# Performance work log

Hardware: AMD Instinct MI355X
Metric: run time of the kernel (lower is better)

The kernel has to match this reference:

```python
import jax, jax.numpy as jnp
import numpy as np

DIM = 256
HEADS = 8
SPLIT = 7
IDX = 0  # H_sp = H, W_sp = split_size
SCALE = (DIM // HEADS) ** -0.5


def setup_inputs() -> dict:
    key = jax.random.key(0)
    k1, k2, k3 = jax.random.split(key, 3)
    B, H, W = 16, 56, 56
    L = H * W
    qkv = jax.random.normal(k1, (3, B, L, DIM), jnp.float32)
    get_v_w = jax.random.normal(k2, (DIM, 1, 3, 3), jnp.float32) * 0.1
    get_v_b = jax.random.normal(k3, (DIM,), jnp.float32) * 0.1
    return {"qkv": qkv, "get_v_w": get_v_w, "get_v_b": get_v_b, "H": H, "W": W}


def reference(qkv, get_v_w, get_v_b, H, W):
    q, k, v = qkv[0], qkv[1], qkv[2]
    B, L, C = q.shape
    Hs, Ws = H, SPLIT  # idx == 0 branch
    hd = C // HEADS
    win = Hs * Ws
    nW = B * (H // Hs) * (W // Ws)

    def im2cswin(x):
        x = x.reshape(B, H // Hs, Hs, W // Ws, Ws, C)
        x = x.transpose(0, 1, 3, 2, 4, 5).reshape(nW, win, HEADS, hd)
        return x.transpose(0, 2, 1, 3)

    qw = im2cswin(q) * SCALE
    kw = im2cswin(k)

    # LePE: depthwise 3x3 conv applied per window in NCHW layout
    vimg = v.reshape(B, H // Hs, Hs, W // Ws, Ws, C)
    vimg = vimg.transpose(0, 1, 3, 5, 2, 4).reshape(nW, C, Hs, Ws)
    lepe = jax.lax.conv_general_dilated(
        vimg, get_v_w, window_strides=(1, 1), padding='SAME',
        feature_group_count=C,
        dimension_numbers=('NCHW', 'OIHW', 'NCHW'))
    lepe = lepe + get_v_b[None, :, None, None]
    lepe = lepe.reshape(nW, HEADS, hd, win).transpose(0, 1, 3, 2)
    vw = vimg.reshape(nW, HEADS, hd, win).transpose(0, 1, 3, 2)

    attn = jax.nn.softmax(jnp.einsum('whqd,whkd->whqk', qw, kw), axis=-1)
    x = jnp.einsum('whqk,whkd->whqd', attn, vw) + lepe

    # windows -> image -> [B, L, C]
    x = x.transpose(0, 2, 1, 3).reshape(B, H // Hs, W // Ws, Hs, Ws, C)
    x = x.transpose(0, 1, 3, 2, 4, 5).reshape(B, H * W, C)
    return x
```

## Files before the change

### kernel.cpp

```cpp
#include <hip/hip_runtime.h>
#include <hip/hip_bf16.h>


#define NB    16
#define IMGH  56
#define IMGW  56
#define LTOK  3136
#define DIMC  256
#define NHEAD 8
#define HD    32
#define WS    7
#define WIN   392
#define QS    0.17677669529663687f
#define LOG2E 1.4426950408889634f

#define KROWS  416
#define KPITCH 40
#define VPITCH 424
#define NKT    13
#define NQT    13

typedef __attribute__((ext_vector_type(8)))  short short8;
typedef __attribute__((ext_vector_type(16))) float f32x16;

union U4S8 { unsigned u[4]; short8 v; };

__device__ inline short f2bf(float x) {
    __hip_bfloat16 h = __float2bfloat16(x);
    union { __hip_bfloat16 b; short s; } u; u.b = h; return u.s;
}
__device__ inline float bf2f(short s) {
    union { float f; unsigned u; } u;
    u.u = ((unsigned)(unsigned short)s) << 16; return u.f;
}
__device__ inline unsigned pk2(float a, float b) {
    return (unsigned)(unsigned short)f2bf(a) | ((unsigned)(unsigned short)f2bf(b) << 16);
}

#if __has_builtin(__builtin_amdgcn_exp2f)
__device__ inline float exp2v(float x) { return __builtin_amdgcn_exp2f(x); }
#else
__device__ inline float exp2v(float x) {
    float r; asm("v_exp_f32 %0, %1" : "=v"(r) : "v"(x)); return r;
}
#endif

__device__ inline void plswap(unsigned &a, unsigned &b) {
    asm("s_nop 1\n\tv_permlane32_swap_b32 %0, %1" : "+v"(a), "+v"(b));
}
__device__ inline void plswapf(float &a, float &b) {
    asm("s_nop 1\n\tv_permlane32_swap_b32 %0, %1" : "+v"(a), "+v"(b));
}

__global__ __launch_bounds__(512, 4) void lepe_mfma_kernel(
    const float* __restrict__ qkv,
    const float* __restrict__ w9,
    const float* __restrict__ bias,
    float* __restrict__ out)
{
    const int tid  = threadIdx.x;
    const int lane = tid & 63;
    const int wave = tid >> 6;
    const int blk  = blockIdx.x;
    const int hh   = blk & 7;
    const int wi   = blk >> 3;
    const int b    = wi >> 3;
    const int wb   = wi & 7;

    __shared__ __align__(16) short Kb[KROWS * KPITCH];
    __shared__ __align__(16) short Vt[HD * VPITCH];
    __shared__ float Ws9[HD][9];
    __shared__ float Bs[HD];
    __shared__ float InvAll[KROWS];

    {
        const int sub = tid & 7;
        const int rb  = tid >> 3;
        for (int it = 0; it < 7; ++it) {
            const int r = it * 64 + rb;
            if (r < WIN) {
                const int h = r / WS, w = r - h * WS;
                const int l = h * IMGW + wb * WS + w;
                const size_t kb = ((size_t)(NB + b) * LTOK + l) * DIMC + hh * HD + sub * 4;
                const float4 kq = *(const float4*)(qkv + kb);
                const float4 vq = *(const float4*)(qkv + kb + (size_t)NB * LTOK * DIMC);
                short4 ks;
                ks.x = f2bf(kq.x); ks.y = f2bf(kq.y); ks.z = f2bf(kq.z); ks.w = f2bf(kq.w);
                *(short4*)&Kb[r * KPITCH + sub * 4] = ks;
                const int d0 = sub * 4;
                Vt[(d0 + 0) * VPITCH + r] = f2bf(vq.x);
                Vt[(d0 + 1) * VPITCH + r] = f2bf(vq.y);
                Vt[(d0 + 2) * VPITCH + r] = f2bf(vq.z);
                Vt[(d0 + 3) * VPITCH + r] = f2bf(vq.w);
            } else if (r < KROWS) {
                *(short4*)&Kb[r * KPITCH + sub * 4] = make_short4(0, 0, 0, 0);
            }
        }
        for (int i = tid; i < HD * (VPITCH - WIN); i += 512) {
            const int d = i >> 5;
            const int c = WIN + (i & 31);
            Vt[d * VPITCH + c] = 0;
        }
        for (int i = tid; i < HD * 9; i += 512)
            Ws9[i / 9][i % 9] = w9[(hh * HD + i / 9) * 9 + (i % 9)];
        if (tid < HD) Bs[tid] = bias[hh * HD + tid];
    }
    __syncthreads();

    const int cq = lane & 31;
    const int hi = lane >> 5;

    f32x16 accA, accB;

    auto attn = [&](int qt, f32x16 &acc) {
        int qtok = qt * 32 + cq; if (qtok > WIN - 1) qtok = WIN - 1;
        const int qh = qtok / WS, qw = qtok - qh * WS;
        const int ql = qh * IMGW + wb * WS + qw;
        const float* qp = qkv + ((size_t)b * LTOK + ql) * DIMC + hh * HD;
        const float qs = QS * LOG2E;
        const float4 qa = *(const float4*)(qp + hi * 8);
        const float4 qb = *(const float4*)(qp + hi * 8 + 4);
        const float4 qc = *(const float4*)(qp + 16 + hi * 8);
        const float4 qd = *(const float4*)(qp + 16 + hi * 8 + 4);
        U4S8 qf0, qf1;
        qf0.u[0] = pk2(qa.x * qs, qa.y * qs);
        qf0.u[1] = pk2(qa.z * qs, qa.w * qs);
        qf0.u[2] = pk2(qb.x * qs, qb.y * qs);
        qf0.u[3] = pk2(qb.z * qs, qb.w * qs);
        qf1.u[0] = pk2(qc.x * qs, qc.y * qs);
        qf1.u[1] = pk2(qc.z * qs, qc.w * qs);
        qf1.u[2] = pk2(qd.x * qs, qd.y * qs);
        qf1.u[3] = pk2(qd.z * qs, qd.w * qs);

        #pragma unroll
        for (int i = 0; i < 16; ++i) acc[i] = 0.f;
        float lsum = 0.f;

        for (int kt = 0; kt < NKT - 1; ++kt) {
            const short* kr = &Kb[(kt * 32 + cq) * KPITCH];
            const short8 ka0 = *(const short8*)(kr + hi * 8);
            const short8 ka1 = *(const short8*)(kr + 16 + hi * 8);
            const short* vr = &Vt[cq * VPITCH + kt * 32 + hi * 8];
            const short8 vb0 = *(const short8*)vr;
            const short8 vb1 = *(const short8*)(vr + 16);

            f32x16 S;
            #pragma unroll
            for (int i = 0; i < 16; ++i) S[i] = 0.f;
            S = __builtin_amdgcn_mfma_f32_32x32x16_bf16(ka0, qf0.v, S, 0, 0, 0);
            S = __builtin_amdgcn_mfma_f32_32x32x16_bf16(ka1, qf1.v, S, 0, 0, 0);

            float p[16];
            #pragma unroll
            for (int r = 0; r < 16; ++r) { p[r] = exp2v(S[r]); lsum += p[r]; }

            unsigned u0 = pk2(p[0],  p[1]),  u2 = pk2(p[4],  p[5]);
            unsigned u1 = pk2(p[2],  p[3]),  u3 = pk2(p[6],  p[7]);
            plswap(u0, u2);
            plswap(u1, u3);
            U4S8 pa0; pa0.u[0] = u0; pa0.u[1] = u1; pa0.u[2] = u2; pa0.u[3] = u3;
            acc = __builtin_amdgcn_mfma_f32_32x32x16_bf16(pa0.v, vb0, acc, 0, 0, 0);

            unsigned t0 = pk2(p[8],  p[9]),  t2 = pk2(p[12], p[13]);
            unsigned t1 = pk2(p[10], p[11]), t3 = pk2(p[14], p[15]);
            plswap(t0, t2);
            plswap(t1, t3);
            U4S8 pa1; pa1.u[0] = t0; pa1.u[1] = t1; pa1.u[2] = t2; pa1.u[3] = t3;
            acc = __builtin_amdgcn_mfma_f32_32x32x16_bf16(pa1.v, vb1, acc, 0, 0, 0);
        }

        {
            const int kt = NKT - 1;
            const short* kr = &Kb[(kt * 32 + cq) * KPITCH];
            const short8 ka0 = *(const short8*)(kr + hi * 8);
            const short8 ka1 = *(const short8*)(kr + 16 + hi * 8);
            const short* vr = &Vt[cq * VPITCH + kt * 32 + hi * 8];
            const short8 vb0 = *(const short8*)vr;

            f32x16 S;
            #pragma unroll
            for (int i = 0; i < 16; ++i) S[i] = 0.f;
            S = __builtin_amdgcn_mfma_f32_32x32x16_bf16(ka0, qf0.v, S, 0, 0, 0);
            S = __builtin_amdgcn_mfma_f32_32x32x16_bf16(ka1, qf1.v, S, 0, 0, 0);

            const float p0 = exp2v(S[0]), p1 = exp2v(S[1]);
            const float p2 = exp2v(S[2]), p3 = exp2v(S[3]);
            lsum += (p0 + p1) + (p2 + p3);
            unsigned u0 = pk2(p0, p1), u2 = 0u;
            unsigned u1 = pk2(p2, p3), u3 = 0u;
            plswap(u0, u2);
            plswap(u1, u3);
            U4S8 pa0; pa0.u[0] = u0; pa0.u[1] = u1; pa0.u[2] = u2; pa0.u[3] = u3;
            acc = __builtin_amdgcn_mfma_f32_32x32x16_bf16(pa0.v, vb0, acc, 0, 0, 0);
        }

        float s0 = lsum, s1 = lsum;
        plswapf(s0, s1);
        const float inv = 1.0f / (s0 + s1);
        if (hi == 0) InvAll[qt * 32 + cq] = inv;
    };

    attn(wave, accA);
    const int qtB = wave + 8;
    if (qtB < NQT) attn(qtB, accB);
    __syncthreads();

    short* Vs = Kb;
    for (int i = tid; i < WIN * HD; i += 512) {
        const int d = i & 31, t = i >> 5;
        Vs[t * HD + d] = Vt[d * VPITCH + t];
    }
    __syncthreads();

    auto epi = [&](int qt, f32x16 &acc) {
        #pragma unroll
        for (int r = 0; r < 16; ++r) {
            const int qrow = (r & 3) + 8 * (r >> 2) + 4 * hi;
            const int ot = qt * 32 + qrow;
            if (ot < WIN) {
                const float invr = InvAll[ot];
                const int h = ot / WS, w = ot - h * WS;
                float lp = Bs[cq];
                #pragma unroll
                for (int dy = -1; dy <= 1; ++dy) {
                    const int hy = h + dy;
                    if ((unsigned)hy >= (unsigned)IMGH) continue;
                    #pragma unroll
                    for (int dx = -1; dx <= 1; ++dx) {
                        const int wx = w + dx;
                        if ((unsigned)wx >= (unsigned)WS) continue;
                        lp += bf2f(Vs[(hy * WS + wx) * HD + cq]) * Ws9[cq][(dy + 1) * 3 + (dx + 1)];
                    }
                }
                const int l = h * IMGW + wb * WS + w;
                out[((size_t)b * LTOK + l) * DIMC + hh * HD + cq] = acc[r] * invr + lp;
            }
        }
    };

    epi(wave, accA);
    if (qtB < NQT) epi(qtB, accB);
}

extern "C" void kernel_launch(void* const* d_in, const int* in_sizes, int n_in,
                              void* d_out, int out_size, void* d_ws, size_t ws_size,
                              hipStream_t stream) {
    const float* qkv  = (const float*)d_in[0];
    const float* w9   = (const float*)d_in[1];
    const float* bias = (const float*)d_in[2];
    float* out = (float*)d_out;

    dim3 grid(NB * 8 * NHEAD);
    dim3 block(512);
    lepe_mfma_kernel<<<grid, block, 0, stream>>>(qkv, w9, bias, out);
}
```

Baseline: 96.48 us.

## Software-pipeline QK MFMA with exp, hoist Q loads before K/V staging, add setprio

Issues the Q global loads for both query tiles before the K/V shared-memory staging, so their latency overlaps that staging. The attention loop is software-pipelined: the QK^T MFMAs for the next key tile run while exp/pack of the current tile proceeds, and K/V fragments are prefetched one iteration ahead. MFMA issue is wrapped in s_setprio to favour matrix instructions across waves. This costs extra registers (two score tiles, prefetched V and both Q fragment sets live), which may pressure occupancy at 512x4 launch bounds. exp2 now always goes through inline asm v_exp_f32.

```diff
diff --git a/kernel.cpp b/kernel.cpp
--- a/kernel.cpp
+++ b/kernel.cpp
@@ -37,13 +37,9 @@
     return (unsigned)(unsigned short)f2bf(a) | ((unsigned)(unsigned short)f2bf(b) << 16);
 }
 
-#if __has_builtin(__builtin_amdgcn_exp2f)
-__device__ inline float exp2v(float x) { return __builtin_amdgcn_exp2f(x); }
-#else
 __device__ inline float exp2v(float x) {
     float r; asm("v_exp_f32 %0, %1" : "=v"(r) : "v"(x)); return r;
 }
-#endif
 
 __device__ inline void plswap(unsigned &a, unsigned &b) {
     asm("s_nop 1\n\tv_permlane32_swap_b32 %0, %1" : "+v"(a), "+v"(b));
@@ -72,6 +68,30 @@
     __shared__ float Ws9[HD][9];
     __shared__ float Bs[HD];
     __shared__ float InvAll[KROWS];
+
+    const int cq = lane & 31;
+    const int hi = lane >> 5;
+
+    const int qtA = wave;
+    const int qtB = wave + 8;
+    const float qs = QS * LOG2E;
+
+    auto qaddr = [&](int qt) -> const float* {
+        int qtok = qt * 32 + cq; if (qtok > WIN - 1) qtok = WIN - 1;
+        const int qh = qtok / WS, qw = qtok - qh * WS;
+        const int ql = qh * IMGW + wb * WS + qw;
+        return qkv + ((size_t)b * LTOK + ql) * DIMC + hh * HD;
+    };
+    const float* qpA = qaddr(qtA);
+    const float* qpB = qaddr(qtB < NQT ? qtB : NQT - 1);
+    const float4 Aa = *(const float4*)(qpA + hi * 8);
+    const float4 Ab = *(const float4*)(qpA + hi * 8 + 4);
+    const float4 Ac = *(const float4*)(qpA + 16 + hi * 8);
+    const float4 Ad = *(const float4*)(qpA + 16 + hi * 8 + 4);
+    const float4 Ba = *(const float4*)(qpB + hi * 8);
+    const float4 Bb = *(const float4*)(qpB + hi * 8 + 4);
+    const float4 Bc = *(const float4*)(qpB + 16 + hi * 8);
+    const float4 Bd = *(const float4*)(qpB + 16 + hi * 8 + 4);
 
     {
         const int sub = tid & 7;
@@ -105,93 +125,102 @@
             Ws9[i / 9][i % 9] = w9[(hh * HD + i / 9) * 9 + (i % 9)];
         if (tid < HD) Bs[tid] = bias[hh * HD + tid];
     }
+
+    U4S8 qA0, qA1, qB0, qB1;
+    qA0.u[0] = pk2(Aa.x * qs, Aa.y * qs); qA0.u[1] = pk2(Aa.z * qs, Aa.w * qs);
+    qA0.u[2] = pk2(Ab.x * qs, Ab.y * qs); qA0.u[3] = pk2(Ab.z * qs, Ab.w * qs);
+    qA1.u[0] = pk2(Ac.x * qs, Ac.y * qs); qA1.u[1] = pk2(Ac.z * qs, Ac.w * qs);
+    qA1.u[2] = pk2(Ad.x * qs, Ad.y * qs); qA1.u[3] = pk2(Ad.z * qs, Ad.w * qs);
+    qB0.u[0] = pk2(Ba.x * qs, Ba.y * qs); qB0.u[1] = pk2(Ba.z * qs, Ba.w * qs);
+    qB0.u[2] = pk2(Bb.x * qs, Bb.y * qs); qB0.u[3] = pk2(Bb.z * qs, Bb.w * qs);
+    qB1.u[0] = pk2(Bc.x * qs, Bc.y * qs); qB1.u[1] = pk2(Bc.z * qs, Bc.w * qs);
+    qB1.u[2] = pk2(Bd.x * qs, Bd.y * qs); qB1.u[3] = pk2(Bd.z * qs, Bd.w * qs);
+
     __syncthreads();
 
-    const int cq = lane & 31;
-    const int hi = lane >> 5;
-
     f32x16 accA, accB;
 
-    auto attn = [&](int qt, f32x16 &acc) {
-        int qtok = qt * 32 + cq; if (qtok > WIN - 1) qtok = WIN - 1;
-        const int qh = qtok / WS, qw = qtok - qh * WS;
-        const int ql = qh * IMGW + wb * WS + qw;
-        const float* qp = qkv + ((size_t)b * LTOK + ql) * DIMC + hh * HD;
-        const float qs = QS * LOG2E;
-        const float4 qa = *(const float4*)(qp + hi * 8);
-        const float4 qb = *(const float4*)(qp + hi * 8 + 4);
-        const float4 qc = *(const float4*)(qp + 16 + hi * 8);
-        const float4 qd = *(const float4*)(qp + 16 + hi * 8 + 4);
-        U4S8 qf0, qf1;
-        qf0.u[0] = pk2(qa.x * qs, qa.y * qs);
-        qf0.u[1] = pk2(qa.z * qs, qa.w * qs);
-        qf0.u[2] = pk2(qb.x * qs, qb.y * qs);
-        qf0.u[3] = pk2(qb.z * qs, qb.w * qs);
-        qf1.u[0] = pk2(qc.x * qs, qc.y * qs);
-        qf1.u[1] = pk2(qc.z * qs, qc.w * qs);
-        qf1.u[2] = pk2(qd.x * qs, qd.y * qs);
-        qf1.u[3] = pk2(qd.z * qs, qd.w * qs);
-
+    auto attn = [&](int qt, const U4S8 &qf0, const U4S8 &qf1, f32x16 &acc) {
         #pragma unroll
         for (int i = 0; i < 16; ++i) acc[i] = 0.f;
         float lsum = 0.f;
 
-        for (int kt = 0; kt < NKT - 1; ++kt) {
-            const short* kr = &Kb[(kt * 32 + cq) * KPITCH];
+        short8 vb0c, vb1c;
+        f32x16 Scur;
+        {
+            const short* kr = &Kb[(0 * 32 + cq) * KPITCH];
             const short8 ka0 = *(const short8*)(kr + hi * 8);
             const short8 ka1 = *(const short8*)(kr + 16 + hi * 8);
-            const short* vr = &Vt[cq * VPITCH + kt * 32 + hi * 8];
-            const short8 vb0 = *(const short8*)vr;
-            const short8 vb1 = *(const short8*)(vr + 16);
-
-            f32x16 S;
+            const short* vr = &Vt[cq * VPITCH + 0 * 32 + hi * 8];
+            vb0c = *(const short8*)vr;
+            vb1c = *(const short8*)(vr + 16);
             #pragma unroll
-            for (int i = 0; i < 16; ++i) S[i] = 0.f;
-            S = __builtin_amdgcn_mfma_f32_32x32x16_bf16(ka0, qf0.v, S, 0, 0, 0);
-            S = __builtin_amdgcn_mfma_f32_32x32x16_bf16(ka1, qf1.v, S, 0, 0, 0);
-
-            float p[16];
+            for (int i = 0; i < 16; ++i) Scur[i] = 0.f;
+            __builtin_amdgcn_s_setprio(1);
+            Scur = __builtin_amdgcn_mfma_f32_32x32x16_bf16(ka0, qf0.v, Scur, 0, 0, 0);
+            Scur = __builtin_amdgcn_mfma_f32_32x32x16_bf16(ka1, qf1.v, Scur, 0, 0, 0);
+            __builtin_amdgcn_s_setprio(0);
+        }
+
+        #pragma unroll 2
+        for (int kt = 0; kt < NKT - 1; ++kt) {
+            const short* kr = &Kb[((kt + 1) * 32 + cq) * KPITCH];
+            const short8 ka0 = *(const short8*)(kr + hi * 8);
+            const short8 ka1 = *(const short8*)(kr + 16 + hi * 8);
+            const short* vr = &Vt[cq * VPITCH + (kt + 1) * 32 + hi * 8];
+            const short8 vb0n = *(const short8*)vr;
+            const short8 vb1n = *(const short8*)(vr + 16);
+            f32x16 Sn;
             #pragma unroll
-            for (int r = 0; r < 16; ++r) { p[r] = exp2v(S[r]); lsum += p[r]; }
-
-            unsigned u0 = pk2(p[0],  p[1]),  u2 = pk2(p[4],  p[5]);
-            unsigned u1 = pk2(p[2],  p[3]),  u3 = pk2(p[6],  p[7]);
+            for (int i = 0; i < 16; ++i) Sn[i] = 0.f;
+            __builtin_amdgcn_s_setprio(1);
+            Sn = __builtin_amdgcn_mfma_f32_32x32x16_bf16(ka0, qf0.v, Sn, 0, 0, 0);
+            Sn = __builtin_amdgcn_mfma_f32_32x32x16_bf16(ka1, qf1.v, Sn, 0, 0, 0);
+            __builtin_amdgcn_s_setprio(0);
+
+            const float p0 = exp2v(Scur[0]), p1 = exp2v(Scur[1]);
+            const float p2 = exp2v(Scur[2]), p3 = exp2v(Scur[3]);
+            const float p4 = exp2v(Scur[4]), p5 = exp2v(Scur[5]);
+            const float p6 = exp2v(Scur[6]), p7 = exp2v(Scur[7]);
+            lsum += ((p0 + p1) + (p2 + p3)) + ((p4 + p5) + (p6 + p7));
+            unsigned u0 = pk2(p0, p1), u2 = pk2(p4, p5);
+            unsigned u1 = pk2(p2, p3), u3 = pk2(p6, p7);
             plswap(u0, u2);
             plswap(u1, u3);
             U4S8 pa0; pa0.u[0] = u0; pa0.u[1] = u1; pa0.u[2] = u2; pa0.u[3] = u3;
-            acc = __builtin_amdgcn_mfma_f32_32x32x16_bf16(pa0.v, vb0, acc, 0, 0, 0);
-
-            unsigned t0 = pk2(p[8],  p[9]),  t2 = pk2(p[12], p[13]);
-            unsigned t1 = pk2(p[10], p[11]), t3 = pk2(p[14], p[15]);
+            __builtin_amdgcn_s_setprio(1);
+            acc = __builtin_amdgcn_mfma_f32_32x32x16_bf16(pa0.v, vb0c, acc, 0, 0, 0);
+            __builtin_amdgcn_s_setprio(0);
+
+            const float p8 = exp2v(Scur[8]),  p9 = exp2v(Scur[9]);
+            const float pa = exp2v(Scur[10]), pb = exp2v(Scur[11]);
+            const float pc = exp2v(Scur[12]), pd = exp2v(Scur[13]);
+            const float pe = exp2v(Scur[14]), pf = exp2v(Scur[15]);
+            lsum += ((p8 + p9) + (pa + pb)) + ((pc + pd) + (pe + pf));
+            unsigned t0 = pk2(p8, p9), t2 = pk2(pc, pd);
+            unsigned t1 = pk2(pa, pb), t3 = pk2(pe, pf);
             plswap(t0, t2);
             plswap(t1, t3);
             U4S8 pa1; pa1.u[0] = t0; pa1.u[1] = t1; pa1.u[2] = t2; pa1.u[3] = t3;
-            acc = __builtin_amdgcn_mfma_f32_32x32x16_bf16(pa1.v, vb1, acc, 0, 0, 0);
+            __builtin_amdgcn_s_setprio(1);
+            acc = __builtin_amdgcn_mfma_f32_32x32x16_bf16(pa1.v, vb1c, acc, 0, 0, 0);
+            __builtin_amdgcn_s_setprio(0);
+
+            Scur = Sn; vb0c = vb0n; vb1c = vb1n;
         }
 
         {
-            const int kt = NKT - 1;
-            const short* kr = &Kb[(kt * 32 + cq) * KPITCH];
-            const short8 ka0 = *(const short8*)(kr + hi * 8);
-            const short8 ka1 = *(const short8*)(kr + 16 + hi * 8);
-            const short* vr = &Vt[cq * VPITCH + kt * 32 + hi * 8];
-            const short8 vb0 = *(const short8*)vr;
-
-            f32x16 S;
-            #pragma unroll
-            for (int i = 0; i < 16; ++i) S[i] = 0.f;
-            S = __builtin_amdgcn_mfma_f32_32x32x16_bf16(ka0, qf0.v, S, 0, 0, 0);
-            S = __builtin_amdgcn_mfma_f32_32x32x16_bf16(ka1, qf1.v, S, 0, 0, 0);
-
-            const float p0 = exp2v(S[0]), p1 = exp2v(S[1]);
-            const float p2 = exp2v(S[2]), p3 = exp2v(S[3]);
+            const float p0 = exp2v(Scur[0]), p1 = exp2v(Scur[1]);
+            const float p2 = exp2v(Scur[2]), p3 = exp2v(Scur[3]);
             lsum += (p0 + p1) + (p2 + p3);
             unsigned u0 = pk2(p0, p1), u2 = 0u;
             unsigned u1 = pk2(p2, p3), u3 = 0u;
             plswap(u0, u2);
             plswap(u1, u3);
             U4S8 pa0; pa0.u[0] = u0; pa0.u[1] = u1; pa0.u[2] = u2; pa0.u[3] = u3;
-            acc = __builtin_amdgcn_mfma_f32_32x32x16_bf16(pa0.v, vb0, acc, 0, 0, 0);
+            __builtin_amdgcn_s_setprio(1);
+            acc = __builtin_amdgcn_mfma_f32_32x32x16_bf16(pa0.v, vb0c, acc, 0, 0, 0);
+            __builtin_amdgcn_s_setprio(0);
         }
 
         float s0 = lsum, s1 = lsum;
@@ -200,9 +229,8 @@
         if (hi == 0) InvAll[qt * 32 + cq] = inv;
     };
 
-    attn(wave, accA);
-    const int qtB = wave + 8;
-    if (qtB < NQT) attn(qtB, accB);
+    attn(qtA, qA0, qA1, accA);
+    if (qtB < NQT) attn(qtB, qB0, qB1, accB);
     __syncthreads();
 
     short* Vs = Kb;
@@ -238,7 +266,7 @@
         }
     };
 
-    epi(wave, accA);
+    epi(qtA, accA);
     if (qtB < NQT) epi(qtB, accB);
 }
 
```

Result: slower. 99.32 us (median of 2 runs) (+2.9%).
